# Kernel tuning notes

Measured on AMD Instinct MI355X. Metric: run time of the kernel, lower is better.

## Reference

```python
import jax, jax.numpy as jnp
import numpy as np

B, TQ, TK = 8, 256, 256
DQ, DK, DV, H = 512, 512, 512, 256


def setup_inputs() -> dict:
    key = jax.random.key(0)
    k1, k2, k3, k4, k5, k6 = jax.random.split(key, 6)
    queries = jax.random.normal(k1, (B, TQ, DQ), dtype=jnp.float32)
    keys = jax.random.normal(k2, (B, TK, DK), dtype=jnp.float32)
    values = jax.random.normal(k3, (B, TK, DV), dtype=jnp.float32)
    # Linear(in, out, bias=False): y = x @ W.T with W (out,in); store transposed (in,out)
    Wq = jax.random.normal(k4, (DQ, H), dtype=jnp.float32) / np.sqrt(DQ)
    Wk = jax.random.normal(k5, (DK, H), dtype=jnp.float32) / np.sqrt(DK)
    wv = jax.random.normal(k6, (H,), dtype=jnp.float32) / np.sqrt(H)
    return {"queries": queries, "keys": keys, "values": values,
            "Wq": Wq, "Wk": Wk, "wv": wv}


def reference(queries, keys, values, Wq, Wk, wv):
    q = jnp.einsum('bqd,dh->bqh', queries, Wq)          # (B,Tq,H)
    k = jnp.einsum('bkd,dh->bkh', keys, Wk)             # (B,Tk,H)
    features = jnp.tanh(q[:, :, None, :] + k[:, None, :, :])  # (B,Tq,Tk,H)
    scores = jnp.einsum('bqkh,h->bqk', features, wv)    # (B,Tq,Tk)
    attn = jax.nn.softmax(scores, axis=-1)              # (B,Tq,Tk)
    return jnp.einsum('bqk,bkv->bqv', attn, values)     # (B,Tq,Dv)
```

## Files before the change

### kernel.cpp

```cpp
#include <hip/hip_runtime.h>

typedef float v2f __attribute__((ext_vector_type(2)));
typedef short bf16x8 __attribute__((ext_vector_type(8)));
typedef float f32x4 __attribute__((ext_vector_type(4)));

namespace {
constexpr int B   = 8;
constexpr int TQ  = 256;
constexpr int TK  = 256;
constexpr int DQK = 512;
constexpr int DV  = 512;
constexpr int H   = 256;
constexpr int QB  = 4;
constexpr float C2LOG2E   = 2.8853900817779268f;
constexpr float NEG2LOG2E = -2.8853900817779268f;
}

__device__ __forceinline__ uint32_t f2u(float x) { return __builtin_bit_cast(uint32_t, x); }
__device__ __forceinline__ float u2f(uint32_t x) { return __builtin_bit_cast(float, x); }
__device__ __forceinline__ uint32_t pack_hi(float x, float y) {
    return (f2u(y) & 0xFFFF0000u) | (f2u(x) >> 16);
}

__global__ __launch_bounds__(256)
void proj_kernel(const float* __restrict__ Q, const float* __restrict__ Kin,
                 const float* __restrict__ Wq, const float* __restrict__ Wk,
                 float* __restrict__ qpc, float* __restrict__ kpc4)
{
    __shared__ short Ahi[4][64][8];
    __shared__ short Alo[4][64][8];
    __shared__ short Bhi[4][32][8];
    __shared__ short Blo[4][32][8];

    const bool kside = (blockIdx.z == 1);
    const float* A = kside ? Kin : Q;
    const float* W = kside ? Wk  : Wq;
    const int m0 = blockIdx.x * 64;
    const int n0 = blockIdx.y * 32;
    const int tid = threadIdx.x;

    const int am = tid >> 2, ag = tid & 3;
    const int bk = tid >> 3, bn4 = (tid & 7) * 4;
    const float4* aptr = (const float4*)(A + (m0 + am) * DQK) + ag * 2;
    const float*  wptr = W + bk * H + n0 + bn4;

    const int w = tid >> 6, l = tid & 63;
    const int wm = (w >> 1) * 32, wn = (w & 1) * 16;
    const int fg = l >> 4;
    const int fr = l & 15;

    float4 a0 = aptr[0], a1 = aptr[1];
    float4 bv = *(const float4*)wptr;

    f32x4 acc0 = {0.f, 0.f, 0.f, 0.f};
    f32x4 acc1 = {0.f, 0.f, 0.f, 0.f};

    for (int s = 0; s < 16; ++s) {
        __syncthreads();
        {
            float ah0 = u2f(f2u(a0.x) & 0xFFFF0000u), ah1 = u2f(f2u(a0.y) & 0xFFFF0000u);
            float ah2 = u2f(f2u(a0.z) & 0xFFFF0000u), ah3 = u2f(f2u(a0.w) & 0xFFFF0000u);
            float ah4 = u2f(f2u(a1.x) & 0xFFFF0000u), ah5 = u2f(f2u(a1.y) & 0xFFFF0000u);
            float ah6 = u2f(f2u(a1.z) & 0xFFFF0000u), ah7 = u2f(f2u(a1.w) & 0xFFFF0000u);
            int4 hw, lw;
            hw.x = (int)pack_hi(a0.x, a0.y); hw.y = (int)pack_hi(a0.z, a0.w);
            hw.z = (int)pack_hi(a1.x, a1.y); hw.w = (int)pack_hi(a1.z, a1.w);
            lw.x = (int)pack_hi(a0.x - ah0, a0.y - ah1);
            lw.y = (int)pack_hi(a0.z - ah2, a0.w - ah3);
            lw.z = (int)pack_hi(a1.x - ah4, a1.y - ah5);
            lw.w = (int)pack_hi(a1.z - ah6, a1.w - ah7);
            *(int4*)&Ahi[ag][am][0] = hw;
            *(int4*)&Alo[ag][am][0] = lw;
            const int g = bk >> 3, slot = bk & 7;
            float bb[4] = {bv.x, bv.y, bv.z, bv.w};
            #pragma unroll
            for (int i = 0; i < 4; ++i) {
                uint32_t u = f2u(bb[i]);
                float hf = u2f(u & 0xFFFF0000u);
                Bhi[g][bn4 + i][slot] = (short)(u >> 16);
                Blo[g][bn4 + i][slot] = (short)(f2u(bb[i] - hf) >> 16);
            }
        }
        __syncthreads();
        if (s < 15) {
            a0 = aptr[s * 8 + 8];
            a1 = aptr[s * 8 + 9];
            bv = *(const float4*)(wptr + (s + 1) * 32 * H);
        }
        bf16x8 ah_0 = *(const bf16x8*)&Ahi[fg][wm + fr][0];
        bf16x8 ah_1 = *(const bf16x8*)&Ahi[fg][wm + 16 + fr][0];
        bf16x8 al_0 = *(const bf16x8*)&Alo[fg][wm + fr][0];
        bf16x8 al_1 = *(const bf16x8*)&Alo[fg][wm + 16 + fr][0];
        bf16x8 bh   = *(const bf16x8*)&Bhi[fg][wn + fr][0];
        bf16x8 bl   = *(const bf16x8*)&Blo[fg][wn + fr][0];
        acc0 = __builtin_amdgcn_mfma_f32_16x16x32_bf16(ah_0, bh, acc0, 0, 0, 0);
        acc1 = __builtin_amdgcn_mfma_f32_16x16x32_bf16(ah_1, bh, acc1, 0, 0, 0);
        acc0 = __builtin_amdgcn_mfma_f32_16x16x32_bf16(ah_0, bl, acc0, 0, 0, 0);
        acc1 = __builtin_amdgcn_mfma_f32_16x16x32_bf16(ah_1, bl, acc1, 0, 0, 0);
        acc0 = __builtin_amdgcn_mfma_f32_16x16x32_bf16(al_0, bh, acc0, 0, 0, 0);
        acc1 = __builtin_amdgcn_mfma_f32_16x16x32_bf16(al_1, bh, acc1, 0, 0, 0);
    }

    const int col = n0 + wn + fr;
    #pragma unroll
    for (int mi = 0; mi < 2; ++mi) {
        f32x4 acc = mi ? acc1 : acc0;
        #pragma unroll
        for (int r = 0; r < 4; ++r) {
            const int row = m0 + wm + mi * 16 + fg * 4 + r;
            float val = __builtin_amdgcn_exp2f(acc[r] * C2LOG2E);
            if (!kside) {
                qpc[row * H + col] = val;
            } else {
                const int bb2 = row >> 8, kk = row & 255;
                kpc4[((bb2 * (H / 4) + (col >> 2)) * TK + kk) * 4 + (col & 3)] = val;
            }
        }
    }
}

__global__ __launch_bounds__(512)
void attn_kernel(const float* __restrict__ qpc, const float* __restrict__ kpc4,
                 const float* __restrict__ wv, const float* __restrict__ values,
                 float* __restrict__ out)
{
    __shared__ float qlds[H][QB];
    __shared__ float wlds[H];
    __shared__ float accbuf[4][QB][TK];
    __shared__ float pT[TK][QB];
    __shared__ float rowsum[QB];

    const int b   = blockIdx.x >> 6;
    const int q0  = (blockIdx.x & 63) * QB;
    const int tid = threadIdx.x;

    for (int i = tid; i < QB * H; i += 512) {
        const int h = i >> 2, q = i & 3;
        qlds[h][q] = qpc[(b * TQ + q0 + q) * H + h];
    }
    if (tid < H) wlds[tid] = wv[tid];
    __syncthreads();

    {
        const int kp = tid & 127;
        const int hg = tid >> 7;
        const int h0 = hg * 64;
        const float4* kc = (const float4*)kpc4 + (b * (H / 4) + (h0 >> 2)) * TK + 2 * kp;
        v2f a01a = {0.f, 0.f}, a23a = {0.f, 0.f};
        v2f a01b = {0.f, 0.f}, a23b = {0.f, 0.f};
        const v2f one = {1.0f, 1.0f};
        float4 kva4 = kc[0];
        float4 kvb4 = kc[1];
        #pragma unroll
        for (int h4 = 0; h4 < 16; ++h4) {
            float4 nkva, nkvb;
            if (h4 < 15) {
                nkva = kc[(h4 + 1) * TK];
                nkvb = kc[(h4 + 1) * TK + 1];
            }
            float4 w4 = *(const float4*)&wlds[h0 + h4 * 4];
            #pragma unroll
            for (int j = 0; j < 4; ++j) {
                const int h = h0 + h4 * 4 + j;
                const float ea = (j == 0) ? kva4.x : (j == 1) ? kva4.y : (j == 2) ? kva4.z : kva4.w;
                const float eb = (j == 0) ? kvb4.x : (j == 1) ? kvb4.y : (j == 2) ? kvb4.z : kvb4.w;
                const float wj = (j == 0) ? w4.x  : (j == 1) ? w4.y  : (j == 2) ? w4.z  : w4.w;
                float4 qa = *(const float4*)&qlds[h][0];
                v2f q01 = {qa.x, qa.y}, q23 = {qa.z, qa.w};
                v2f ea2 = {ea, ea}, eb2 = {eb, eb}, w2 = {wj, wj};
                v2f d0a = __builtin_elementwise_fma(q01, ea2, one);
                v2f d1a = __builtin_elementwise_fma(q23, ea2, one);
                v2f d0b = __builtin_elementwise_fma(q01, eb2, one);
                v2f d1b = __builtin_elementwise_fma(q23, eb2, one);
                v2f r0a, r1a, r0b, r1b;
                r0a.x = __builtin_amdgcn_rcpf(d0a.x);
                r0a.y = __builtin_amdgcn_rcpf(d0a.y);
                r1a.x = __builtin_amdgcn_rcpf(d1a.x);
                r1a.y = __builtin_amdgcn_rcpf(d1a.y);
                r0b.x = __builtin_amdgcn_rcpf(d0b.x);
                r0b.y = __builtin_amdgcn_rcpf(d0b.y);
                r1b.x = __builtin_amdgcn_rcpf(d1b.x);
                r1b.y = __builtin_amdgcn_rcpf(d1b.y);
                a01a = __builtin_elementwise_fma(w2, r0a, a01a);
                a23a = __builtin_elementwise_fma(w2, r1a, a23a);
                a01b = __builtin_elementwise_fma(w2, r0b, a01b);
                a23b = __builtin_elementwise_fma(w2, r1b, a23b);
            }
            kva4 = nkva;
            kvb4 = nkvb;
        }
        accbuf[hg][0][2 * kp]     = a01a.x;
        accbuf[hg][1][2 * kp]     = a01a.y;
        accbuf[hg][2][2 * kp]     = a23a.x;
        accbuf[hg][3][2 * kp]     = a23a.y;
        accbuf[hg][0][2 * kp + 1] = a01b.x;
        accbuf[hg][1][2 * kp + 1] = a01b.y;
        accbuf[hg][2][2 * kp + 1] = a23b.x;
        accbuf[hg][3][2 * kp + 1] = a23b.y;
    }
    __syncthreads();

    for (int i = tid; i < QB * TK; i += 512) {
        const int kk = i >> 2, q = i & 3;
        float s = (accbuf[0][q][kk] + accbuf[1][q][kk]) +
                  (accbuf[2][q][kk] + accbuf[3][q][kk]);
        pT[kk][q] = __builtin_amdgcn_exp2f(s * NEG2LOG2E);
    }
    __syncthreads();

    {
        const int q = (tid >> 6) & 3, lane = tid & 63;
        float s = (pT[lane][q] + pT[lane + 64][q]) +
                  (pT[lane + 128][q] + pT[lane + 192][q]);
        #pragma unroll
        for (int off = 1; off < 64; off <<= 1)
            s += __shfl_xor(s, off);
        if (tid < 256 && lane == 0) rowsum[q] = s;
    }

    {
        const int c = tid;
        const float* vb = values + b * TK * DV + c;
        v2f o01 = {0.f, 0.f}, o23 = {0.f, 0.f};
        #pragma unroll 8
        for (int kk = 0; kk < TK; ++kk) {
            float v = vb[kk * DV];
            float4 p4 = *(const float4*)&pT[kk][0];
            v2f vv = {v, v};
            o01 = __builtin_elementwise_fma((v2f){p4.x, p4.y}, vv, o01);
            o23 = __builtin_elementwise_fma((v2f){p4.z, p4.w}, vv, o23);
        }
        __syncthreads();
        float* ob = out + (b * TQ + q0) * DV + c;
        ob[0 * DV] = o01.x * __builtin_amdgcn_rcpf(rowsum[0]);
        ob[1 * DV] = o01.y * __builtin_amdgcn_rcpf(rowsum[1]);
        ob[2 * DV] = o23.x * __builtin_amdgcn_rcpf(rowsum[2]);
        ob[3 * DV] = o23.y * __builtin_amdgcn_rcpf(rowsum[3]);
    }
}

extern "C" void kernel_launch(void* const* d_in, const int* in_sizes, int n_in,
                              void* d_out, int out_size, void* d_ws, size_t ws_size,
                              hipStream_t stream)
{
    const float* queries = (const float*)d_in[0];
    const float* keys    = (const float*)d_in[1];
    const float* values  = (const float*)d_in[2];
    const float* Wq      = (const float*)d_in[3];
    const float* Wk      = (const float*)d_in[4];
    const float* wv      = (const float*)d_in[5];
    float* out  = (float*)d_out;
    float* qpc  = (float*)d_ws;
    float* kpc4 = qpc + B * TQ * H;

    dim3 gproj(B * TQ / 64, H / 32, 2);
    proj_kernel<<<gproj, 256, 0, stream>>>(queries, keys, Wq, Wk, qpc, kpc4);
    attn_kernel<<<B * (TQ / QB), 512, 0, stream>>>(qpc, kpc4, wv, values, out);
}
```

Baseline: 49.42 us.

## Double query block per attention workgroup and drop cross-thread H reduction

Raises the queries per block from 4 to 8, halving the grid and doubling reuse of each loaded value row in the PV product. Each thread now owns one key and four queries across all of H, so the shared-memory partial-sum buffer and its extra barrier and reduction pass go away, and exp is applied directly. Per-thread serial work over H grows fourfold, and the grid drops to 256 blocks, which may underfill the GPU. Launch bounds now request two blocks per CU.

```diff
diff --git a/kernel.cpp b/kernel.cpp
--- a/kernel.cpp
+++ b/kernel.cpp
@@ -11,7 +11,7 @@
 constexpr int DQK = 512;
 constexpr int DV  = 512;
 constexpr int H   = 256;
-constexpr int QB  = 4;
+constexpr int QB  = 8;
 constexpr float C2LOG2E   = 2.8853900817779268f;
 constexpr float NEG2LOG2E = -2.8853900817779268f;
 }
@@ -119,116 +119,93 @@
     }
 }
 
-__global__ __launch_bounds__(512)
+__global__ __launch_bounds__(512, 2)
 void attn_kernel(const float* __restrict__ qpc, const float* __restrict__ kpc4,
                  const float* __restrict__ wv, const float* __restrict__ values,
                  float* __restrict__ out)
 {
     __shared__ float qlds[H][QB];
     __shared__ float wlds[H];
-    __shared__ float accbuf[4][QB][TK];
     __shared__ float pT[TK][QB];
     __shared__ float rowsum[QB];
 
-    const int b   = blockIdx.x >> 6;
-    const int q0  = (blockIdx.x & 63) * QB;
+    const int b   = blockIdx.x >> 5;
+    const int q0  = (blockIdx.x & 31) * QB;
     const int tid = threadIdx.x;
 
     for (int i = tid; i < QB * H; i += 512) {
-        const int h = i >> 2, q = i & 3;
+        const int q = i >> 8, h = i & 255;
         qlds[h][q] = qpc[(b * TQ + q0 + q) * H + h];
     }
     if (tid < H) wlds[tid] = wv[tid];
     __syncthreads();
 
     {
-        const int kp = tid & 127;
-        const int hg = tid >> 7;
-        const int h0 = hg * 64;
-        const float4* kc = (const float4*)kpc4 + (b * (H / 4) + (h0 >> 2)) * TK + 2 * kp;
-        v2f a01a = {0.f, 0.f}, a23a = {0.f, 0.f};
-        v2f a01b = {0.f, 0.f}, a23b = {0.f, 0.f};
+        const int k  = tid & 255;
+        const int qh = tid >> 8;
+        const float4* kc = (const float4*)kpc4 + (b * (H / 4)) * TK + k;
+        v2f a01 = {0.f, 0.f}, a23 = {0.f, 0.f};
         const v2f one = {1.0f, 1.0f};
-        float4 kva4 = kc[0];
-        float4 kvb4 = kc[1];
-        #pragma unroll
-        for (int h4 = 0; h4 < 16; ++h4) {
-            float4 nkva, nkvb;
-            if (h4 < 15) {
-                nkva = kc[(h4 + 1) * TK];
-                nkvb = kc[(h4 + 1) * TK + 1];
-            }
-            float4 w4 = *(const float4*)&wlds[h0 + h4 * 4];
+        float4 kv = kc[0];
+        #pragma unroll 8
+        for (int h4 = 0; h4 < 64; ++h4) {
+            float4 nkv;
+            if (h4 < 63) nkv = kc[(h4 + 1) * TK];
+            float4 w4 = *(const float4*)&wlds[h4 * 4];
             #pragma unroll
             for (int j = 0; j < 4; ++j) {
-                const int h = h0 + h4 * 4 + j;
-                const float ea = (j == 0) ? kva4.x : (j == 1) ? kva4.y : (j == 2) ? kva4.z : kva4.w;
-                const float eb = (j == 0) ? kvb4.x : (j == 1) ? kvb4.y : (j == 2) ? kvb4.z : kvb4.w;
-                const float wj = (j == 0) ? w4.x  : (j == 1) ? w4.y  : (j == 2) ? w4.z  : w4.w;
-                float4 qa = *(const float4*)&qlds[h][0];
-                v2f q01 = {qa.x, qa.y}, q23 = {qa.z, qa.w};
-                v2f ea2 = {ea, ea}, eb2 = {eb, eb}, w2 = {wj, wj};
-                v2f d0a = __builtin_elementwise_fma(q01, ea2, one);
-                v2f d1a = __builtin_elementwise_fma(q23, ea2, one);
-                v2f d0b = __builtin_elementwise_fma(q01, eb2, one);
-                v2f d1b = __builtin_elementwise_fma(q23, eb2, one);
-                v2f r0a, r1a, r0b, r1b;
-                r0a.x = __builtin_amdgcn_rcpf(d0a.x);
-                r0a.y = __builtin_amdgcn_rcpf(d0a.y);
-                r1a.x = __builtin_amdgcn_rcpf(d1a.x);
-                r1a.y = __builtin_amdgcn_rcpf(d1a.y);
-                r0b.x = __builtin_amdgcn_rcpf(d0b.x);
-                r0b.y = __builtin_amdgcn_rcpf(d0b.y);
-                r1b.x = __builtin_amdgcn_rcpf(d1b.x);
-                r1b.y = __builtin_amdgcn_rcpf(d1b.y);
-                a01a = __builtin_elementwise_fma(w2, r0a, a01a);
-                a23a = __builtin_elementwise_fma(w2, r1a, a23a);
-                a01b = __builtin_elementwise_fma(w2, r0b, a01b);
-                a23b = __builtin_elementwise_fma(w2, r1b, a23b);
+                const int h = h4 * 4 + j;
+                const float ek = (j == 0) ? kv.x : (j == 1) ? kv.y : (j == 2) ? kv.z : kv.w;
+                const float wj = (j == 0) ? w4.x : (j == 1) ? w4.y : (j == 2) ? w4.z : w4.w;
+                float4 qa = *(const float4*)&qlds[h][4 * qh];
+                v2f ek2 = {ek, ek}, w2 = {wj, wj};
+                v2f qp0 = {qa.x, qa.y}, qp1 = {qa.z, qa.w};
+                v2f d0 = __builtin_elementwise_fma(qp0, ek2, one);
+                v2f d1 = __builtin_elementwise_fma(qp1, ek2, one);
+                v2f r0, r1;
+                r0.x = __builtin_amdgcn_rcpf(d0.x);
+                r0.y = __builtin_amdgcn_rcpf(d0.y);
+                r1.x = __builtin_amdgcn_rcpf(d1.x);
+                r1.y = __builtin_amdgcn_rcpf(d1.y);
+                a01 = __builtin_elementwise_fma(w2, r0, a01);
+                a23 = __builtin_elementwise_fma(w2, r1, a23);
             }
-            kva4 = nkva;
-            kvb4 = nkvb;
-        }
-        accbuf[hg][0][2 * kp]     = a01a.x;
-        accbuf[hg][1][2 * kp]     = a01a.y;
-        accbuf[hg][2][2 * kp]     = a23a.x;
-        accbuf[hg][3][2 * kp]     = a23a.y;
-        accbuf[hg][0][2 * kp + 1] = a01b.x;
-        accbuf[hg][1][2 * kp + 1] = a01b.y;
-        accbuf[hg][2][2 * kp + 1] = a23b.x;
-        accbuf[hg][3][2 * kp + 1] = a23b.y;
+            kv = nkv;
+        }
+        float4 e;
+        e.x = __builtin_amdgcn_exp2f(a01.x * NEG2LOG2E);
+        e.y = __builtin_amdgcn_exp2f(a01.y * NEG2LOG2E);
+        e.z = __builtin_amdgcn_exp2f(a23.x * NEG2LOG2E);
+        e.w = __builtin_amdgcn_exp2f(a23.y * NEG2LOG2E);
+        *(float4*)&pT[k][4 * qh] = e;
     }
     __syncthreads();
 
-    for (int i = tid; i < QB * TK; i += 512) {
-        const int kk = i >> 2, q = i & 3;
-        float s = (accbuf[0][q][kk] + accbuf[1][q][kk]) +
-                  (accbuf[2][q][kk] + accbuf[3][q][kk]);
-        pT[kk][q] = __builtin_amdgcn_exp2f(s * NEG2LOG2E);
-    }
-    __syncthreads();
-
     {
-        const int q = (tid >> 6) & 3, lane = tid & 63;
+        const int q = tid >> 6, lane = tid & 63;
         float s = (pT[lane][q] + pT[lane + 64][q]) +
                   (pT[lane + 128][q] + pT[lane + 192][q]);
         #pragma unroll
         for (int off = 1; off < 64; off <<= 1)
             s += __shfl_xor(s, off);
-        if (tid < 256 && lane == 0) rowsum[q] = s;
+        if (lane == 0) rowsum[q] = s;
     }
 
     {
         const int c = tid;
         const float* vb = values + b * TK * DV + c;
         v2f o01 = {0.f, 0.f}, o23 = {0.f, 0.f};
+        v2f o45 = {0.f, 0.f}, o67 = {0.f, 0.f};
         #pragma unroll 8
         for (int kk = 0; kk < TK; ++kk) {
             float v = vb[kk * DV];
-            float4 p4 = *(const float4*)&pT[kk][0];
+            float4 p4a = *(const float4*)&pT[kk][0];
+            float4 p4b = *(const float4*)&pT[kk][4];
             v2f vv = {v, v};
-            o01 = __builtin_elementwise_fma((v2f){p4.x, p4.y}, vv, o01);
-            o23 = __builtin_elementwise_fma((v2f){p4.z, p4.w}, vv, o23);
+            o01 = __builtin_elementwise_fma((v2f){p4a.x, p4a.y}, vv, o01);
+            o23 = __builtin_elementwise_fma((v2f){p4a.z, p4a.w}, vv, o23);
+            o45 = __builtin_elementwise_fma((v2f){p4b.x, p4b.y}, vv, o45);
+            o67 = __builtin_elementwise_fma((v2f){p4b.z, p4b.w}, vv, o67);
         }
         __syncthreads();
         float* ob = out + (b * TQ + q0) * DV + c;
@@ -236,6 +213,10 @@
         ob[1 * DV] = o01.y * __builtin_amdgcn_rcpf(rowsum[1]);
         ob[2 * DV] = o23.x * __builtin_amdgcn_rcpf(rowsum[2]);
         ob[3 * DV] = o23.y * __builtin_amdgcn_rcpf(rowsum[3]);
+        ob[4 * DV] = o45.x * __builtin_amdgcn_rcpf(rowsum[4]);
+        ob[5 * DV] = o45.y * __builtin_amdgcn_rcpf(rowsum[5]);
+        ob[6 * DV] = o67.x * __builtin_amdgcn_rcpf(rowsum[6]);
+        ob[7 * DV] = o67.y * __builtin_amdgcn_rcpf(rowsum[7]);
     }
 }
 
```

After: 50.42 us. +2.0%, slower.
